# Kernel tuning notes

Measured on AMD Instinct MI355X. Metric: run time of the kernel, lower is better.

## Reference

```python
import jax, jax.numpy as jnp
import numpy as np

EMBED_DIM = 512
N_HEADS = 8
HEAD_DIM = EMBED_DIM // N_HEADS


def setup_inputs() -> dict:
    key = jax.random.key(0)
    ks = jax.random.split(key, 5)
    B, N, D = 2, 4096, EMBED_DIM
    scale = 1.0 / np.sqrt(D)
    x = jax.random.normal(ks[0], (B, N, D), dtype=jnp.float32)
    W_qkv = jax.random.normal(ks[1], (D, 3 * D), dtype=jnp.float32) * scale
    b_qkv = jnp.zeros((3 * D,), dtype=jnp.float32)
    W_out = jax.random.normal(ks[2], (D, D), dtype=jnp.float32) * scale
    b_out = jnp.zeros((D,), dtype=jnp.float32)
    return {"x": x, "W_qkv": W_qkv, "b_qkv": b_qkv, "W_out": W_out, "b_out": b_out}


def reference(x, W_qkv, b_qkv, W_out, b_out):
    B, N, D = x.shape
    H, Hd = N_HEADS, HEAD_DIM
    qkv = x @ W_qkv + b_qkv                      # [B, N, 3D]
    q, k, v = jnp.split(qkv, 3, axis=-1)
    # [B, N, D] -> [B, H, N, Hd]
    q = q.reshape(B, N, H, Hd).transpose(0, 2, 1, 3)
    k = k.reshape(B, N, H, Hd).transpose(0, 2, 1, 3)
    v = v.reshape(B, N, H, Hd).transpose(0, 2, 1, 3)
    scores = jnp.einsum('bhqd,bhkd->bhqk', q, k) / np.sqrt(Hd)  # [B, H, N, N]
    attn = jax.nn.softmax(scores, axis=-1)
    out = jnp.einsum('bhqk,bhkd->bhqd', attn, v)  # [B, H, N, Hd]
    out = out.transpose(0, 2, 1, 3).reshape(B, N, D)
    return out @ W_out + b_out
```

## Files before the change

### kernel.cpp

```cpp
#include <hip/hip_runtime.h>

typedef __attribute__((ext_vector_type(4))) float f32x4;
typedef __attribute__((ext_vector_type(8))) __bf16 bf16x8;
typedef __attribute__((ext_vector_type(4))) __bf16 bf16x4;
typedef __attribute__((ext_vector_type(4))) short s16x4;

#define DEVI static __device__ __forceinline__

#define LOG2E 1.44269504088896340736f
#define THR 10.0f

DEVI short f2bf(float f) {
  return __builtin_bit_cast(short, (__bf16)f);
}

DEVI void gll16(const short* gsrc, short* ldst) {
  __builtin_amdgcn_global_load_lds(
      (const __attribute__((address_space(1))) unsigned*)gsrc,
      (__attribute__((address_space(3))) unsigned*)ldst, 16, 0, 0);
}

DEVI void stage_gran(const short* g, int ldRow, short* lds, int p, int lane) {
  int q = p + lane;
  int row = q >> 3;
  int k8 = (q & 7) ^ (row & 7);
  gll16(g + (size_t)row * ldRow + k8 * 8, lds + (size_t)p * 8);
}

DEVI bf16x8 frag_ld(const short* base, int lane, int kk) {
  int r = lane & 15;
  int chunk = (kk * 4 + (lane >> 4)) ^ (r & 7);
  return *(const bf16x8*)(base + r * 64 + chunk * 8);
}


__global__ void cvt_k(const float* __restrict__ in, short* __restrict__ out, int n4) {
  int i = blockIdx.x * blockDim.x + threadIdx.x;
  if (i < n4) {
    f32x4 v = *(const f32x4*)(in + (size_t)i * 4);
    s16x4 o;
    #pragma unroll
    for (int j = 0; j < 4; ++j) o[j] = f2bf(v[j]);
    *(s16x4*)(out + (size_t)i * 4) = o;
  }
}

__global__ void tcvt_k(const float* __restrict__ in, short* __restrict__ out, int R, int C) {
  __shared__ float t[32][33];
  const int bx = blockIdx.x * 32;
  const int by = blockIdx.y * 32;
  const int lx = threadIdx.x & 31, ly = threadIdx.x >> 5;
  #pragma unroll
  for (int rr = ly; rr < 32; rr += 8)
    t[rr][lx] = in[(size_t)(by + rr) * C + bx + lx];
  __syncthreads();
  #pragma unroll
  for (int cc = ly; cc < 32; cc += 8)
    out[(size_t)(bx + cc) * R + by + lx] = f2bf(t[lx][cc]);
}


template <int EPI>
__global__ __launch_bounds__(256, 3)
void gemm_k(const short* __restrict__ A, const short* __restrict__ Bt,
            const float* __restrict__ bias, float* __restrict__ outF,
            short* __restrict__ Qb, short* __restrict__ Kb, short* __restrict__ Vtb,
            int M, int N, int K) {
  __shared__ __align__(16) short As[128 * 64];
  __shared__ __align__(16) short Bs[128 * 64];
  const int lane = threadIdx.x & 63;
  const int wid  = threadIdx.x >> 6;
  const int mt = blockIdx.x * 128;
  const int nt = blockIdx.y * 128;
  const int wm = (wid >> 1) * 64;
  const int wn = (wid & 1) * 64;

  f32x4 acc[4][4];
  #pragma unroll
  for (int i = 0; i < 4; ++i)
    #pragma unroll
    for (int j = 0; j < 4; ++j) acc[i][j] = (f32x4){0.f, 0.f, 0.f, 0.f};

  const short* Atile = A + (size_t)mt * K;
  const short* Btile = Bt + (size_t)nt * K;
  const int nkt = K >> 6;

  for (int kt = 0; kt < nkt; ++kt) {
    __syncthreads();
    #pragma unroll
    for (int i = 0; i < 4; ++i) {
      stage_gran(Atile + kt * 64, K, As, (wid * 4 + i) * 64, lane);
      stage_gran(Btile + kt * 64, K, Bs, (wid * 4 + i) * 64, lane);
    }
    __syncthreads();
    #pragma unroll
    for (int kk = 0; kk < 2; ++kk) {
      bf16x8 af[4], bfr[4];
      #pragma unroll
      for (int i = 0; i < 4; ++i) af[i] = frag_ld(As + (wm + i * 16) * 64, lane, kk);
      #pragma unroll
      for (int j = 0; j < 4; ++j) bfr[j] = frag_ld(Bs + (wn + j * 16) * 64, lane, kk);
      #pragma unroll
      for (int i = 0; i < 4; ++i)
        #pragma unroll
        for (int j = 0; j < 4; ++j)
          acc[i][j] = __builtin_amdgcn_mfma_f32_16x16x32_bf16(af[i], bfr[j], acc[i][j], 0, 0, 0);
    }
  }

  const int rbase = (lane >> 4) * 4;
  const int cl = lane & 15;
  #pragma unroll
  for (int i = 0; i < 4; ++i) {
    #pragma unroll
    for (int j = 0; j < 4; ++j) {
      const int col = nt + wn + j * 16 + cl;
      const float bv = bias[col];
      #pragma unroll
      for (int r = 0; r < 4; ++r) {
        const int row = mt + wm + i * 16 + rbase + r;
        float v = acc[i][j][r] + bv;
        if (EPI == 1) {
          outF[(size_t)row * N + col] = v;
        } else {
          const int which = col >> 9;
          const int d = col & 511;
          const int h = d >> 6, hd = d & 63;
          const int b = row >> 12, n = row & 4095;
          const int bh = b * 8 + h;
          if (which == 0)
            Qb[((size_t)bh * 4096 + n) * 64 + hd] = f2bf(v * (0.125f * LOG2E));
          else if (which == 1)
            Kb[((size_t)bh * 4096 + n) * 64 + hd] = f2bf(v);
          else
            Vtb[((size_t)bh * 64 + hd) * 4096 + n] = f2bf(v);
        }
      }
    }
  }
}


__global__ __launch_bounds__(256, 2)
void attn_k(const short* __restrict__ Qb, const short* __restrict__ Kb,
            const short* __restrict__ Vtb, short* __restrict__ AOut) {
  __shared__ __align__(16) short Ks[64 * 64];
  __shared__ __align__(16) short Vs[64 * 64];
  __shared__ __align__(16) short Ps[4][32 * 64];
  const int lane = threadIdx.x & 63;
  const int wid = threadIdx.x >> 6;
  const int bh = blockIdx.y;
  const int qt = blockIdx.x * 128 + wid * 32;
  const short* Qh = Qb + (size_t)bh * 4096 * 64;
  const short* Kh = Kb + (size_t)bh * 4096 * 64;
  const short* Vh = Vtb + (size_t)bh * 64 * 4096;
  const int cl = lane & 15, g = lane >> 4;

  bf16x8 qf[2][2];
  #pragma unroll
  for (int i = 0; i < 2; ++i)
    #pragma unroll
    for (int kd = 0; kd < 2; ++kd)
      qf[i][kd] = *(const bf16x8*)(Qh + (size_t)(qt + i * 16 + cl) * 64 + kd * 32 + g * 8);

  f32x4 o[2][4];
  f32x4 lacc[2];
  #pragma unroll
  for (int i = 0; i < 2; ++i) {
    lacc[i] = (f32x4){0.f, 0.f, 0.f, 0.f};
    #pragma unroll
    for (int jd = 0; jd < 4; ++jd) o[i][jd] = (f32x4){0.f, 0.f, 0.f, 0.f};
  }
  float m[2] = {-1e30f, -1e30f};

  bf16x8 ones;
  #pragma unroll
  for (int e = 0; e < 8; ++e) ones[e] = (__bf16)1.0f;

  short* P = (short*)Ps[wid];
  int pwo[2][4];
  #pragma unroll
  for (int i = 0; i < 2; ++i)
    #pragma unroll
    for (int j = 0; j < 4; ++j)
      pwo[i][j] = (i * 16 + cl) * 64 + (((j * 2 + (g >> 1)) ^ (cl & 7)) * 8) + (g & 1) * 4;

  for (int kv = 0; kv < 4096; kv += 64) {
    __syncthreads();
    #pragma unroll
    for (int t = 0; t < 2; ++t) {
      stage_gran(Kh + (size_t)kv * 64, 64, Ks, (wid * 2 + t) * 64, lane);
      stage_gran(Vh + kv, 4096, Vs, (wid * 2 + t) * 64, lane);
    }
    __syncthreads();

    f32x4 s[2][4];
    #pragma unroll
    for (int i = 0; i < 2; ++i)
      #pragma unroll
      for (int j = 0; j < 4; ++j) s[i][j] = (f32x4){0.f, 0.f, 0.f, 0.f};
    #pragma unroll
    for (int kd = 0; kd < 2; ++kd) {
      bf16x8 kf[4];
      #pragma unroll
      for (int j = 0; j < 4; ++j) kf[j] = frag_ld(Ks + j * 16 * 64, lane, kd);
      #pragma unroll
      for (int i = 0; i < 2; ++i)
        #pragma unroll
        for (int j = 0; j < 4; ++j)
          s[i][j] = __builtin_amdgcn_mfma_f32_16x16x32_bf16(kf[j], qf[i][kd], s[i][j], 0, 0, 0);
    }

    float lmax[2];
    #pragma unroll
    for (int i = 0; i < 2; ++i) {
      float a = fmaxf(fmaxf(s[i][0][0], s[i][0][1]), fmaxf(s[i][0][2], s[i][0][3]));
      float b = fmaxf(fmaxf(s[i][1][0], s[i][1][1]), fmaxf(s[i][1][2], s[i][1][3]));
      float c = fmaxf(fmaxf(s[i][2][0], s[i][2][1]), fmaxf(s[i][2][2], s[i][2][3]));
      float d = fmaxf(fmaxf(s[i][3][0], s[i][3][1]), fmaxf(s[i][3][2], s[i][3][3]));
      lmax[i] = fmaxf(fmaxf(a, b), fmaxf(c, d));
    }

    if (!__all((lmax[0] <= m[0] + THR) && (lmax[1] <= m[1] + THR))) {
      #pragma unroll
      for (int i = 0; i < 2; ++i) {
        float mx = lmax[i];
        mx = fmaxf(mx, __shfl_xor(mx, 16));
        mx = fmaxf(mx, __shfl_xor(mx, 32));
        float mnew = fmaxf(m[i], mx);
        float corr = exp2f(m[i] - mnew);
        m[i] = mnew;
        float c[4];
        #pragma unroll
        for (int r = 0; r < 4; ++r) c[r] = __shfl(corr, (g << 2) | r);
        #pragma unroll
        for (int jd = 0; jd < 4; ++jd)
          #pragma unroll
          for (int r = 0; r < 4; ++r) o[i][jd][r] *= c[r];
        #pragma unroll
        for (int r = 0; r < 4; ++r) lacc[i][r] *= c[r];
      }
    }

    #pragma unroll
    for (int i = 0; i < 2; ++i)
      #pragma unroll
      for (int j = 0; j < 4; ++j) {
        bf16x4 pw;
        #pragma unroll
        for (int r = 0; r < 4; ++r) pw[r] = (__bf16)exp2f(s[i][j][r] - m[i]);
        *(bf16x4*)(P + pwo[i][j]) = pw;
      }

    #pragma unroll
    for (int kk = 0; kk < 2; ++kk) {
      bf16x8 pf[2], vf[4];
      #pragma unroll
      for (int i = 0; i < 2; ++i) pf[i] = frag_ld(P + i * 16 * 64, lane, kk);
      #pragma unroll
      for (int jd = 0; jd < 4; ++jd) vf[jd] = frag_ld(Vs + jd * 16 * 64, lane, kk);
      #pragma unroll
      for (int i = 0; i < 2; ++i)
        lacc[i] = __builtin_amdgcn_mfma_f32_16x16x32_bf16(pf[i], ones, lacc[i], 0, 0, 0);
      #pragma unroll
      for (int i = 0; i < 2; ++i)
        #pragma unroll
        for (int jd = 0; jd < 4; ++jd)
          o[i][jd] = __builtin_amdgcn_mfma_f32_16x16x32_bf16(pf[i], vf[jd], o[i][jd], 0, 0, 0);
    }
  }

  const int b = bh >> 3, h = bh & 7;
  #pragma unroll
  for (int i = 0; i < 2; ++i) {
    #pragma unroll
    for (int r = 0; r < 4; ++r) {
      const float inv = 1.f / lacc[i][r];
      const int n = qt + i * 16 + g * 4 + r;
      #pragma unroll
      for (int jd = 0; jd < 4; ++jd) {
        const int d = h * 64 + jd * 16 + cl;
        AOut[((size_t)b * 4096 + n) * 512 + d] = f2bf(o[i][jd][r] * inv);
      }
    }
  }
}


extern "C" void kernel_launch(void* const* d_in, const int* in_sizes, int n_in,
                              void* d_out, int out_size, void* d_ws, size_t ws_size,
                              hipStream_t stream) {
  const float* x    = (const float*)d_in[0];
  const float* Wqkv = (const float*)d_in[1];
  const float* bqkv = (const float*)d_in[2];
  const float* Wout = (const float*)d_in[3];
  const float* bout = (const float*)d_in[4];
  float* out = (float*)d_out;

  short* ws   = (short*)d_ws;
  short* xb   = ws;
  short* Wqt  = xb + 8192 * 512;
  short* Wot  = Wqt + 1536 * 512;
  short* Qb   = Wot + 512 * 512;
  short* Kb   = Qb + 16 * 4096 * 64;
  short* Vtb  = Kb + 16 * 4096 * 64;
  short* AOut = Vtb + 16 * 4096 * 64;

  hipLaunchKernelGGL(cvt_k, dim3(8192 * 512 / 4 / 256), dim3(256), 0, stream,
                     x, xb, 8192 * 512 / 4);
  hipLaunchKernelGGL(tcvt_k, dim3(1536 / 32, 512 / 32), dim3(256), 0, stream,
                     Wqkv, Wqt, 512, 1536);
  hipLaunchKernelGGL(tcvt_k, dim3(512 / 32, 512 / 32), dim3(256), 0, stream,
                     Wout, Wot, 512, 512);
  hipLaunchKernelGGL(gemm_k<0>, dim3(8192 / 128, 1536 / 128), dim3(256), 0, stream,
                     xb, Wqt, bqkv, (float*)nullptr, Qb, Kb, Vtb, 8192, 1536, 512);
  hipLaunchKernelGGL(attn_k, dim3(4096 / 128, 16), dim3(256), 0, stream,
                     Qb, Kb, Vtb, AOut);
  hipLaunchKernelGGL(gemm_k<1>, dim3(8192 / 128, 512 / 128), dim3(256), 0, stream,
                     AOut, Wot, bout, out, (short*)nullptr, (short*)nullptr, (short*)nullptr,
                     8192, 512, 512);
}
```

Measured before the change: 251.0 us.

## Double-buffer K/V tiles in attention, shrink per-wave query tile, raise occupancy

The attention kernel now double-buffers the K and V shared-memory tiles, issuing the next tile's async global-to-LDS loads before computing on the current one, and needs only one barrier per iteration. Each wave handles 16 query rows instead of 32, the grid doubles, and launch bounds request 4 blocks per CU. s_setprio hints are placed around the MFMA phases. This aims to hide load latency and add parallelism, at the cost of halving K/V reuse per block, which doubles K/V traffic from L2.

```diff
diff --git a/kernel.cpp b/kernel.cpp
--- a/kernel.cpp
+++ b/kernel.cpp
@@ -141,147 +141,130 @@
 }
 
 
-__global__ __launch_bounds__(256, 2)
+__global__ __launch_bounds__(256, 4)
 void attn_k(const short* __restrict__ Qb, const short* __restrict__ Kb,
             const short* __restrict__ Vtb, short* __restrict__ AOut) {
-  __shared__ __align__(16) short Ks[64 * 64];
-  __shared__ __align__(16) short Vs[64 * 64];
-  __shared__ __align__(16) short Ps[4][32 * 64];
+  __shared__ __align__(16) short Ks[2][64 * 64];
+  __shared__ __align__(16) short Vs[2][64 * 64];
+  __shared__ __align__(16) short Ps[4][16 * 64];
   const int lane = threadIdx.x & 63;
   const int wid = threadIdx.x >> 6;
   const int bh = blockIdx.y;
-  const int qt = blockIdx.x * 128 + wid * 32;
+  const int qt = blockIdx.x * 64 + wid * 16;
   const short* Qh = Qb + (size_t)bh * 4096 * 64;
   const short* Kh = Kb + (size_t)bh * 4096 * 64;
   const short* Vh = Vtb + (size_t)bh * 64 * 4096;
   const int cl = lane & 15, g = lane >> 4;
 
-  bf16x8 qf[2][2];
-  #pragma unroll
-  for (int i = 0; i < 2; ++i)
-    #pragma unroll
-    for (int kd = 0; kd < 2; ++kd)
-      qf[i][kd] = *(const bf16x8*)(Qh + (size_t)(qt + i * 16 + cl) * 64 + kd * 32 + g * 8);
-
-  f32x4 o[2][4];
-  f32x4 lacc[2];
-  #pragma unroll
-  for (int i = 0; i < 2; ++i) {
-    lacc[i] = (f32x4){0.f, 0.f, 0.f, 0.f};
-    #pragma unroll
-    for (int jd = 0; jd < 4; ++jd) o[i][jd] = (f32x4){0.f, 0.f, 0.f, 0.f};
-  }
-  float m[2] = {-1e30f, -1e30f};
+  bf16x8 qf[2];
+  #pragma unroll
+  for (int kd = 0; kd < 2; ++kd)
+    qf[kd] = *(const bf16x8*)(Qh + (size_t)(qt + cl) * 64 + kd * 32 + g * 8);
+
+  f32x4 o[4];
+  f32x4 lacc = (f32x4){0.f, 0.f, 0.f, 0.f};
+  #pragma unroll
+  for (int jd = 0; jd < 4; ++jd) o[jd] = (f32x4){0.f, 0.f, 0.f, 0.f};
+  float m = -1e30f;
 
   bf16x8 ones;
   #pragma unroll
   for (int e = 0; e < 8; ++e) ones[e] = (__bf16)1.0f;
 
   short* P = (short*)Ps[wid];
-  int pwo[2][4];
-  #pragma unroll
-  for (int i = 0; i < 2; ++i)
-    #pragma unroll
-    for (int j = 0; j < 4; ++j)
-      pwo[i][j] = (i * 16 + cl) * 64 + (((j * 2 + (g >> 1)) ^ (cl & 7)) * 8) + (g & 1) * 4;
-
-  for (int kv = 0; kv < 4096; kv += 64) {
-    __syncthreads();
+  int pwo[4];
+  #pragma unroll
+  for (int j = 0; j < 4; ++j)
+    pwo[j] = cl * 64 + (((j * 2 + (g >> 1)) ^ (cl & 7)) * 8) + (g & 1) * 4;
+
+  auto STAGE = [&](int b, int kv) {
     #pragma unroll
     for (int t = 0; t < 2; ++t) {
-      stage_gran(Kh + (size_t)kv * 64, 64, Ks, (wid * 2 + t) * 64, lane);
-      stage_gran(Vh + kv, 4096, Vs, (wid * 2 + t) * 64, lane);
-    }
-    __syncthreads();
-
-    f32x4 s[2][4];
-    #pragma unroll
-    for (int i = 0; i < 2; ++i)
-      #pragma unroll
-      for (int j = 0; j < 4; ++j) s[i][j] = (f32x4){0.f, 0.f, 0.f, 0.f};
+      stage_gran(Kh + (size_t)kv * 64, 64, Ks[b], (wid * 2 + t) * 64, lane);
+      stage_gran(Vh + kv, 4096, Vs[b], (wid * 2 + t) * 64, lane);
+    }
+  };
+
+  STAGE(0, 0);
+  __syncthreads();
+
+  for (int t = 0; t < 64; ++t) {
+    const int cur = t & 1;
+    if (t < 63) STAGE(cur ^ 1, (t + 1) * 64);
+
+    f32x4 s[4];
+    #pragma unroll
+    for (int j = 0; j < 4; ++j) s[j] = (f32x4){0.f, 0.f, 0.f, 0.f};
+    __builtin_amdgcn_s_setprio(1);
     #pragma unroll
     for (int kd = 0; kd < 2; ++kd) {
       bf16x8 kf[4];
       #pragma unroll
-      for (int j = 0; j < 4; ++j) kf[j] = frag_ld(Ks + j * 16 * 64, lane, kd);
-      #pragma unroll
-      for (int i = 0; i < 2; ++i)
+      for (int j = 0; j < 4; ++j) kf[j] = frag_ld(Ks[cur] + j * 16 * 64, lane, kd);
+      #pragma unroll
+      for (int j = 0; j < 4; ++j)
+        s[j] = __builtin_amdgcn_mfma_f32_16x16x32_bf16(kf[j], qf[kd], s[j], 0, 0, 0);
+    }
+    __builtin_amdgcn_s_setprio(0);
+
+    float a0 = fmaxf(fmaxf(s[0][0], s[0][1]), fmaxf(s[0][2], s[0][3]));
+    float a1 = fmaxf(fmaxf(s[1][0], s[1][1]), fmaxf(s[1][2], s[1][3]));
+    float a2 = fmaxf(fmaxf(s[2][0], s[2][1]), fmaxf(s[2][2], s[2][3]));
+    float a3 = fmaxf(fmaxf(s[3][0], s[3][1]), fmaxf(s[3][2], s[3][3]));
+    float lmax = fmaxf(fmaxf(a0, a1), fmaxf(a2, a3));
+
+    if (!__all(lmax <= m + THR)) {
+      float mx = lmax;
+      mx = fmaxf(mx, __shfl_xor(mx, 16));
+      mx = fmaxf(mx, __shfl_xor(mx, 32));
+      float mnew = fmaxf(m, mx);
+      float corr = exp2f(m - mnew);
+      m = mnew;
+      float c[4];
+      #pragma unroll
+      for (int r = 0; r < 4; ++r) c[r] = __shfl(corr, (g << 2) | r);
+      #pragma unroll
+      for (int jd = 0; jd < 4; ++jd)
         #pragma unroll
-        for (int j = 0; j < 4; ++j)
-          s[i][j] = __builtin_amdgcn_mfma_f32_16x16x32_bf16(kf[j], qf[i][kd], s[i][j], 0, 0, 0);
-    }
-
-    float lmax[2];
-    #pragma unroll
-    for (int i = 0; i < 2; ++i) {
-      float a = fmaxf(fmaxf(s[i][0][0], s[i][0][1]), fmaxf(s[i][0][2], s[i][0][3]));
-      float b = fmaxf(fmaxf(s[i][1][0], s[i][1][1]), fmaxf(s[i][1][2], s[i][1][3]));
-      float c = fmaxf(fmaxf(s[i][2][0], s[i][2][1]), fmaxf(s[i][2][2], s[i][2][3]));
-      float d = fmaxf(fmaxf(s[i][3][0], s[i][3][1]), fmaxf(s[i][3][2], s[i][3][3]));
-      lmax[i] = fmaxf(fmaxf(a, b), fmaxf(c, d));
-    }
-
-    if (!__all((lmax[0] <= m[0] + THR) && (lmax[1] <= m[1] + THR))) {
-      #pragma unroll
-      for (int i = 0; i < 2; ++i) {
-        float mx = lmax[i];
-        mx = fmaxf(mx, __shfl_xor(mx, 16));
-        mx = fmaxf(mx, __shfl_xor(mx, 32));
-        float mnew = fmaxf(m[i], mx);
-        float corr = exp2f(m[i] - mnew);
-        m[i] = mnew;
-        float c[4];
-        #pragma unroll
-        for (int r = 0; r < 4; ++r) c[r] = __shfl(corr, (g << 2) | r);
-        #pragma unroll
-        for (int jd = 0; jd < 4; ++jd)
-          #pragma unroll
-          for (int r = 0; r < 4; ++r) o[i][jd][r] *= c[r];
-        #pragma unroll
-        for (int r = 0; r < 4; ++r) lacc[i][r] *= c[r];
-      }
-    }
-
-    #pragma unroll
-    for (int i = 0; i < 2; ++i)
-      #pragma unroll
-      for (int j = 0; j < 4; ++j) {
-        bf16x4 pw;
-        #pragma unroll
-        for (int r = 0; r < 4; ++r) pw[r] = (__bf16)exp2f(s[i][j][r] - m[i]);
-        *(bf16x4*)(P + pwo[i][j]) = pw;
-      }
-
+        for (int r = 0; r < 4; ++r) o[jd][r] *= c[r];
+      #pragma unroll
+      for (int r = 0; r < 4; ++r) lacc[r] *= c[r];
+    }
+
+    #pragma unroll
+    for (int j = 0; j < 4; ++j) {
+      bf16x4 pw;
+      #pragma unroll
+      for (int r = 0; r < 4; ++r) pw[r] = (__bf16)exp2f(s[j][r] - m);
+      *(bf16x4*)(P + pwo[j]) = pw;
+    }
+
+    __builtin_amdgcn_s_setprio(1);
     #pragma unroll
     for (int kk = 0; kk < 2; ++kk) {
-      bf16x8 pf[2], vf[4];
-      #pragma unroll
-      for (int i = 0; i < 2; ++i) pf[i] = frag_ld(P + i * 16 * 64, lane, kk);
-      #pragma unroll
-      for (int jd = 0; jd < 4; ++jd) vf[jd] = frag_ld(Vs + jd * 16 * 64, lane, kk);
-      #pragma unroll
-      for (int i = 0; i < 2; ++i)
-        lacc[i] = __builtin_amdgcn_mfma_f32_16x16x32_bf16(pf[i], ones, lacc[i], 0, 0, 0);
-      #pragma unroll
-      for (int i = 0; i < 2; ++i)
-        #pragma unroll
-        for (int jd = 0; jd < 4; ++jd)
-          o[i][jd] = __builtin_amdgcn_mfma_f32_16x16x32_bf16(pf[i], vf[jd], o[i][jd], 0, 0, 0);
-    }
+      bf16x8 pf = frag_ld(P, lane, kk);
+      bf16x8 vf[4];
+      #pragma unroll
+      for (int jd = 0; jd < 4; ++jd) vf[jd] = frag_ld(Vs[cur] + jd * 16 * 64, lane, kk);
+      lacc = __builtin_amdgcn_mfma_f32_16x16x32_bf16(pf, ones, lacc, 0, 0, 0);
+      #pragma unroll
+      for (int jd = 0; jd < 4; ++jd)
+        o[jd] = __builtin_amdgcn_mfma_f32_16x16x32_bf16(pf, vf[jd], o[jd], 0, 0, 0);
+    }
+    __builtin_amdgcn_s_setprio(0);
+
+    __syncthreads();
   }
 
   const int b = bh >> 3, h = bh & 7;
   #pragma unroll
-  for (int i = 0; i < 2; ++i) {
-    #pragma unroll
-    for (int r = 0; r < 4; ++r) {
-      const float inv = 1.f / lacc[i][r];
-      const int n = qt + i * 16 + g * 4 + r;
-      #pragma unroll
-      for (int jd = 0; jd < 4; ++jd) {
-        const int d = h * 64 + jd * 16 + cl;
-        AOut[((size_t)b * 4096 + n) * 512 + d] = f2bf(o[i][jd][r] * inv);
-      }
+  for (int r = 0; r < 4; ++r) {
+    const float inv = 1.f / lacc[r];
+    const int n = qt + g * 4 + r;
+    #pragma unroll
+    for (int jd = 0; jd < 4; ++jd) {
+      const int d = h * 64 + jd * 16 + cl;
+      AOut[((size_t)b * 4096 + n) * 512 + d] = f2bf(o[jd][r] * inv);
     }
   }
 }
@@ -314,7 +297,7 @@
                      Wout, Wot, 512, 512);
   hipLaunchKernelGGL(gemm_k<0>, dim3(8192 / 128, 1536 / 128), dim3(256), 0, stream,
                      xb, Wqt, bqkv, (float*)nullptr, Qb, Kb, Vtb, 8192, 1536, 512);
-  hipLaunchKernelGGL(attn_k, dim3(4096 / 128, 16), dim3(256), 0, stream,
+  hipLaunchKernelGGL(attn_k, dim3(4096 / 64, 16), dim3(256), 0, stream,
                      Qb, Kb, Vtb, AOut);
   hipLaunchKernelGGL(gemm_k<1>, dim3(8192 / 128, 512 / 128), dim3(256), 0, stream,
                      AOut, Wot, bout, out, (short*)nullptr, (short*)nullptr, (short*)nullptr,
```

Result: faster. 242.6 us (-3.3%).

## Software-pipeline attention loop with double-buffered K and triple-buffered V tiles

Applied to the files above, without the earlier changes.

Restructures the KV loop so the next K/V tiles are prefetched into alternate LDS buffers (two for K, three for V) while the current tile is computed. QK^T for tile i is skewed against softmax and PV for tile i-1, which cuts the loop down to one barrier per iteration. MFMA sections are wrapped in s_setprio raises to favour matrix issue across waves. The extra buffers raise LDS use to about 56KB per block, which could limit occupancy.

```diff
diff --git a/kernel.cpp b/kernel.cpp
--- a/kernel.cpp
+++ b/kernel.cpp
@@ -144,8 +144,8 @@
 __global__ __launch_bounds__(256, 2)
 void attn_k(const short* __restrict__ Qb, const short* __restrict__ Kb,
             const short* __restrict__ Vtb, short* __restrict__ AOut) {
-  __shared__ __align__(16) short Ks[64 * 64];
-  __shared__ __align__(16) short Vs[64 * 64];
+  __shared__ __align__(16) short Ks[2][64 * 64];
+  __shared__ __align__(16) short Vs[3][64 * 64];
   __shared__ __align__(16) short Ps[4][32 * 64];
   const int lane = threadIdx.x & 63;
   const int wid = threadIdx.x >> 6;
@@ -185,89 +185,120 @@
     for (int j = 0; j < 4; ++j)
       pwo[i][j] = (i * 16 + cl) * 64 + (((j * 2 + (g >> 1)) ^ (cl & 7)) * 8) + (g & 1) * 4;
 
-  for (int kv = 0; kv < 4096; kv += 64) {
-    __syncthreads();
-    #pragma unroll
-    for (int t = 0; t < 2; ++t) {
-      stage_gran(Kh + (size_t)kv * 64, 64, Ks, (wid * 2 + t) * 64, lane);
-      stage_gran(Vh + kv, 4096, Vs, (wid * 2 + t) * 64, lane);
-    }
-    __syncthreads();
-
-    f32x4 s[2][4];
-    #pragma unroll
-    for (int i = 0; i < 2; ++i)
-      #pragma unroll
-      for (int j = 0; j < 4; ++j) s[i][j] = (f32x4){0.f, 0.f, 0.f, 0.f};
-    #pragma unroll
-    for (int kd = 0; kd < 2; ++kd) {
-      bf16x8 kf[4];
-      #pragma unroll
-      for (int j = 0; j < 4; ++j) kf[j] = frag_ld(Ks + j * 16 * 64, lane, kd);
-      #pragma unroll
-      for (int i = 0; i < 2; ++i)
-        #pragma unroll
-        for (int j = 0; j < 4; ++j)
-          s[i][j] = __builtin_amdgcn_mfma_f32_16x16x32_bf16(kf[j], qf[i][kd], s[i][j], 0, 0, 0);
-    }
-
-    float lmax[2];
-    #pragma unroll
-    for (int i = 0; i < 2; ++i) {
-      float a = fmaxf(fmaxf(s[i][0][0], s[i][0][1]), fmaxf(s[i][0][2], s[i][0][3]));
-      float b = fmaxf(fmaxf(s[i][1][0], s[i][1][1]), fmaxf(s[i][1][2], s[i][1][3]));
-      float c = fmaxf(fmaxf(s[i][2][0], s[i][2][1]), fmaxf(s[i][2][2], s[i][2][3]));
-      float d = fmaxf(fmaxf(s[i][3][0], s[i][3][1]), fmaxf(s[i][3][2], s[i][3][3]));
-      lmax[i] = fmaxf(fmaxf(a, b), fmaxf(c, d));
-    }
-
-    if (!__all((lmax[0] <= m[0] + THR) && (lmax[1] <= m[1] + THR))) {
-      #pragma unroll
-      for (int i = 0; i < 2; ++i) {
-        float mx = lmax[i];
-        mx = fmaxf(mx, __shfl_xor(mx, 16));
-        mx = fmaxf(mx, __shfl_xor(mx, 32));
-        float mnew = fmaxf(m[i], mx);
-        float corr = exp2f(m[i] - mnew);
-        m[i] = mnew;
-        float c[4];
-        #pragma unroll
-        for (int r = 0; r < 4; ++r) c[r] = __shfl(corr, (g << 2) | r);
+  auto STAGEK = [&](int b, int kv) {
+    #pragma unroll
+    for (int t = 0; t < 2; ++t)
+      stage_gran(Kh + (size_t)kv * 64, 64, Ks[b], (wid * 2 + t) * 64, lane);
+  };
+  auto STAGEV = [&](int b, int kv) {
+    #pragma unroll
+    for (int t = 0; t < 2; ++t)
+      stage_gran(Vh + kv, 4096, Vs[b], (wid * 2 + t) * 64, lane);
+  };
+
+  STAGEK(0, 0);
+  STAGEV(0, 0);
+  __syncthreads();
+
+  f32x4 s[2][4];
+  int vprev = 2, vcur = 0, vnext = 1;
+
+  for (int i = 0; i <= 64; ++i) {
+    const int kcur = i & 1;
+    if (i < 63) {
+      STAGEK(kcur ^ 1, (i + 1) * 64);
+      STAGEV(vnext, (i + 1) * 64);
+    }
+
+    if (i > 0) {
+      bf16x8 vf[2][4];
+      #pragma unroll
+      for (int kk = 0; kk < 2; ++kk)
         #pragma unroll
         for (int jd = 0; jd < 4; ++jd)
-          #pragma unroll
-          for (int r = 0; r < 4; ++r) o[i][jd][r] *= c[r];
-        #pragma unroll
-        for (int r = 0; r < 4; ++r) lacc[i][r] *= c[r];
-      }
-    }
-
-    #pragma unroll
-    for (int i = 0; i < 2; ++i)
-      #pragma unroll
-      for (int j = 0; j < 4; ++j) {
-        bf16x4 pw;
-        #pragma unroll
-        for (int r = 0; r < 4; ++r) pw[r] = (__bf16)exp2f(s[i][j][r] - m[i]);
-        *(bf16x4*)(P + pwo[i][j]) = pw;
-      }
-
-    #pragma unroll
-    for (int kk = 0; kk < 2; ++kk) {
-      bf16x8 pf[2], vf[4];
-      #pragma unroll
-      for (int i = 0; i < 2; ++i) pf[i] = frag_ld(P + i * 16 * 64, lane, kk);
-      #pragma unroll
-      for (int jd = 0; jd < 4; ++jd) vf[jd] = frag_ld(Vs + jd * 16 * 64, lane, kk);
-      #pragma unroll
-      for (int i = 0; i < 2; ++i)
-        lacc[i] = __builtin_amdgcn_mfma_f32_16x16x32_bf16(pf[i], ones, lacc[i], 0, 0, 0);
-      #pragma unroll
-      for (int i = 0; i < 2; ++i)
-        #pragma unroll
-        for (int jd = 0; jd < 4; ++jd)
-          o[i][jd] = __builtin_amdgcn_mfma_f32_16x16x32_bf16(pf[i], vf[jd], o[i][jd], 0, 0, 0);
-    }
+          vf[kk][jd] = frag_ld(Vs[vprev] + jd * 16 * 64, lane, kk);
+
+      float lmax[2];
+      #pragma unroll
+      for (int i2 = 0; i2 < 2; ++i2) {
+        float a = fmaxf(fmaxf(s[i2][0][0], s[i2][0][1]), fmaxf(s[i2][0][2], s[i2][0][3]));
+        float b = fmaxf(fmaxf(s[i2][1][0], s[i2][1][1]), fmaxf(s[i2][1][2], s[i2][1][3]));
+        float c = fmaxf(fmaxf(s[i2][2][0], s[i2][2][1]), fmaxf(s[i2][2][2], s[i2][2][3]));
+        float d = fmaxf(fmaxf(s[i2][3][0], s[i2][3][1]), fmaxf(s[i2][3][2], s[i2][3][3]));
+        lmax[i2] = fmaxf(fmaxf(a, b), fmaxf(c, d));
+      }
+
+      if (!__all((lmax[0] <= m[0] + THR) && (lmax[1] <= m[1] + THR))) {
+        #pragma unroll
+        for (int i2 = 0; i2 < 2; ++i2) {
+          float mx = lmax[i2];
+          mx = fmaxf(mx, __shfl_xor(mx, 16));
+          mx = fmaxf(mx, __shfl_xor(mx, 32));
+          float mnew = fmaxf(m[i2], mx);
+          float corr = exp2f(m[i2] - mnew);
+          m[i2] = mnew;
+          float c[4];
+          #pragma unroll
+          for (int r = 0; r < 4; ++r) c[r] = __shfl(corr, (g << 2) | r);
+          #pragma unroll
+          for (int jd = 0; jd < 4; ++jd)
+            #pragma unroll
+            for (int r = 0; r < 4; ++r) o[i2][jd][r] *= c[r];
+          #pragma unroll
+          for (int r = 0; r < 4; ++r) lacc[i2][r] *= c[r];
+        }
+      }
+
+      #pragma unroll
+      for (int i2 = 0; i2 < 2; ++i2)
+        #pragma unroll
+        for (int j = 0; j < 4; ++j) {
+          bf16x4 pw;
+          #pragma unroll
+          for (int r = 0; r < 4; ++r) pw[r] = (__bf16)exp2f(s[i2][j][r] - m[i2]);
+          *(bf16x4*)(P + pwo[i2][j]) = pw;
+        }
+
+      __builtin_amdgcn_s_setprio(1);
+      #pragma unroll
+      for (int kk = 0; kk < 2; ++kk) {
+        bf16x8 pf[2];
+        #pragma unroll
+        for (int i2 = 0; i2 < 2; ++i2) pf[i2] = frag_ld(P + i2 * 16 * 64, lane, kk);
+        #pragma unroll
+        for (int i2 = 0; i2 < 2; ++i2)
+          lacc[i2] = __builtin_amdgcn_mfma_f32_16x16x32_bf16(pf[i2], ones, lacc[i2], 0, 0, 0);
+        #pragma unroll
+        for (int i2 = 0; i2 < 2; ++i2)
+          #pragma unroll
+          for (int jd = 0; jd < 4; ++jd)
+            o[i2][jd] = __builtin_amdgcn_mfma_f32_16x16x32_bf16(pf[i2], vf[kk][jd], o[i2][jd], 0, 0, 0);
+      }
+      __builtin_amdgcn_s_setprio(0);
+    }
+
+    if (i < 64) {
+      #pragma unroll
+      for (int i2 = 0; i2 < 2; ++i2)
+        #pragma unroll
+        for (int j = 0; j < 4; ++j) s[i2][j] = (f32x4){0.f, 0.f, 0.f, 0.f};
+      __builtin_amdgcn_s_setprio(1);
+      #pragma unroll
+      for (int kd = 0; kd < 2; ++kd) {
+        bf16x8 kf[4];
+        #pragma unroll
+        for (int j = 0; j < 4; ++j) kf[j] = frag_ld(Ks[kcur] + j * 16 * 64, lane, kd);
+        #pragma unroll
+        for (int i2 = 0; i2 < 2; ++i2)
+          #pragma unroll
+          for (int j = 0; j < 4; ++j)
+            s[i2][j] = __builtin_amdgcn_mfma_f32_16x16x32_bf16(kf[j], qf[i2][kd], s[i2][j], 0, 0, 0);
+      }
+      __builtin_amdgcn_s_setprio(0);
+      __syncthreads();
+    }
+
+    const int t = vprev; vprev = vcur; vcur = vnext; vnext = t;
   }
 
   const int b = bh >> 3, h = bh & 7;
```

Measured after the change: 244.7 us. -2.5%, faster.
